# Kernel optimization log

Measured on AMD Instinct MI355X. Metric: run time of the kernel, lower is better.

## Reference

```python
import jax, jax.numpy as jnp
import numpy as np

N, E, B, D, Q, C = 50000, 250000, 128, 302, 600, 2000
NEG_SLOPE = 0.2  # PyG GATConv default


def setup_inputs() -> dict:
    key = jax.random.key(0)
    ks = jax.random.split(key, 12)
    x = jax.random.normal(ks[0], (N, D), jnp.float32)
    edges = jax.random.randint(ks[1], (2, E), 0, N, dtype=jnp.int32)
    query = jax.random.normal(ks[2], (B, Q), jnp.float32)
    batch = jnp.sort(jax.random.randint(ks[3], (N,), 0, B, dtype=jnp.int32))
    # GATConv(302, 302, heads=1) params (shared across the 3 applications)
    theta = jax.random.normal(ks[4], (D, D), jnp.float32) / np.float32(np.sqrt(D))
    att_src = jax.random.normal(ks[5], (D,), jnp.float32) * 0.1
    att_dst = jax.random.normal(ks[6], (D,), jnp.float32) * 0.1
    gat_bias = jnp.zeros((D,), jnp.float32)
    # Attention.W ~ torch.rand(decoder_dim, encoder_dim) -> stored as [Q, D]
    attW = jax.random.uniform(ks[7], (Q, D), jnp.float32)
    lin_w = jax.random.normal(ks[8], (C, D), jnp.float32) / np.float32(np.sqrt(D))
    lin_b = jnp.zeros((C,), jnp.float32)
    return {"x": x, "edges": edges, "query": query, "batch": batch,
            "theta": theta, "att_src": att_src, "att_dst": att_dst,
            "gat_bias": gat_bias, "attW": attW, "lin_w": lin_w, "lin_b": lin_b}


def _segment_softmax(s, seg, num_segments):
    m = jax.ops.segment_max(s, seg, num_segments=num_segments)
    ex = jnp.exp(s - m[seg])
    den = jax.ops.segment_sum(ex, seg, num_segments=num_segments)
    return ex / den[seg]


def reference(x, edges, query, batch, theta, att_src, att_dst, gat_bias, attW, lin_w, lin_b):
    # add self loops once (PyG GATConv add_self_loops=True)
    loops = jnp.arange(N, dtype=edges.dtype)
    src = jnp.concatenate([edges[0], loops])
    dst = jnp.concatenate([edges[1], loops])

    def gat(h_in):
        h = h_in @ theta.T                       # [N, D]
        a_s = h @ att_src                        # [N]
        a_d = h @ att_dst                        # [N]
        e = jax.nn.leaky_relu(a_s[src] + a_d[dst], NEG_SLOPE)  # [E+N]
        alpha = _segment_softmax(e, dst, N)      # softmax over incoming edges
        out = jax.ops.segment_sum(alpha[:, None] * h[src], dst, num_segments=N)
        return out + gat_bias

    h = jax.nn.relu(gat(x))
    h = jax.nn.relu(gat(h))
    h = jax.nn.relu(gat(h))                      # [N, D]

    # Attention pooling: score_j = (query[batch_j] @ W) . h_j / sqrt(Q)
    qp = query @ attW                            # [B, D]
    s = jnp.sum(qp[batch] * h, axis=-1) / np.float32(np.sqrt(Q))  # [N]
    w = _segment_softmax(s, batch, B)            # per-graph softmax weights
    pooled = jax.ops.segment_sum(w[:, None] * h, batch, num_segments=B)  # [B, D]

    return jax.nn.relu(pooled) @ lin_w.T + lin_b  # [B, C]
```

## Files before the change

kernel.cpp:

```cpp
#include <hip/hip_runtime.h>
#include <hip/hip_bf16.h>
#include <math.h>

#define N_NODES 50000
#define N_EDGES 250000
#define BB      128
#define DD      302
#define QQ      600
#define CC      2000
#define NEG_SLOPE 0.2f
#define GS      304
#define KP      320
#define KSTEPS  10
#define PC      64
#define BPK_KS  20480

typedef __attribute__((ext_vector_type(8))) short short8;
typedef __attribute__((ext_vector_type(4))) float f32x4;

__device__ __forceinline__ void gload_lds16(const void* g, void* l) {
    __builtin_amdgcn_global_load_lds((const __attribute__((address_space(1))) void*)g,
                                     (__attribute__((address_space(3))) void*)l, 16, 0, 0);
}

__device__ __host__ __forceinline__ int bswz(int q, int n) {
    return q ^ (n & 3) ^ ((n >> 2) & 3);
}

__global__ void k_histogram(const int* __restrict__ dst, int* deg) {
    int e = blockIdx.x * blockDim.x + threadIdx.x;
    if (e < N_EDGES) atomicAdd(&deg[dst[e]], 1);
}

__global__ void k_scan_block(const int* __restrict__ deg, int* offs, int* partials) {
    __shared__ int sh[256];
    int i = blockIdx.x * 256 + threadIdx.x;
    int v = (i < N_NODES) ? deg[i] : 0;
    sh[threadIdx.x] = v;
    __syncthreads();
    for (int d = 1; d < 256; d <<= 1) {
        int t = (threadIdx.x >= d) ? sh[threadIdx.x - d] : 0;
        __syncthreads();
        sh[threadIdx.x] += t;
        __syncthreads();
    }
    if (i < N_NODES) offs[i] = sh[threadIdx.x] - v;
    if (threadIdx.x == 255) partials[blockIdx.x] = sh[255];
}

__global__ void k_scan_partials(int* partials, int nb) {
    __shared__ int sh[256];
    int v = (threadIdx.x < nb) ? partials[threadIdx.x] : 0;
    sh[threadIdx.x] = v;
    __syncthreads();
    for (int d = 1; d < 256; d <<= 1) {
        int t = (threadIdx.x >= d) ? sh[threadIdx.x - d] : 0;
        __syncthreads();
        sh[threadIdx.x] += t;
        __syncthreads();
    }
    if (threadIdx.x < nb) partials[threadIdx.x] = sh[threadIdx.x] - v;
}

__global__ void k_scatter(const int* __restrict__ src, const int* __restrict__ dst,
                          const int* __restrict__ offs, const int* __restrict__ partials,
                          const int* __restrict__ deg, int* cursor, int* esrc) {
    int i = blockIdx.x * blockDim.x + threadIdx.x;
    if (i < N_EDGES) {
        int d = dst[i];
        int base = offs[d] + partials[d >> 8] + d;
        int pos = base + atomicAdd(&cursor[d], 1);
        esrc[pos] = src[i];
    } else if (i < N_EDGES + N_NODES) {
        int n = i - N_EDGES;
        int base = offs[n] + partials[n >> 8] + n;
        esrc[base + deg[n]] = n;
    }
}

__global__ void k_theta_prep(const float* __restrict__ theta,
                             const float* __restrict__ att_src,
                             const float* __restrict__ att_dst,
                             unsigned short* __restrict__ bpk,
                             const float* __restrict__ query,
                             float* __restrict__ qp) {
    if (blockIdx.x >= 402) {
        int t = blockIdx.x - 402;
        int b = t >> 1;
        int d = (t & 1) * 256 + threadIdx.x;
        if (d >= DD) return;
        const float* qrow = query + (size_t)b * QQ;
        float acc = 0.f;
        #pragma unroll 8
        for (int q = 0; q < QQ; q++) acc += qrow[q] * qp[0 * 0] * 0.f + qrow[q] * 0.f;
        return;
    }
    if (blockIdx.x >= 400) {
        int k = (blockIdx.x - 400) * 256 + threadIdx.x;
        if (k >= KP) return;
        float vs = 0.f, vd = 0.f;
        if (k < DD) {
            for (int j = 0; j < DD; j++) {
                float t = theta[j * DD + k];
                vs += t * att_src[j];
                vd += t * att_dst[j];
            }
        }
        int ks = k >> 5, kk = k & 31, q = kk >> 3, kb = kk & 7;
        size_t b0 = (size_t)ks * BPK_KS + DD * 32 + bswz(q, DD) * 8 + kb;
        size_t b1 = (size_t)ks * BPK_KS + (DD + 1) * 32 + bswz(q, DD + 1) * 8 + kb;
        unsigned int u, uh, ul;
        u  = __float_as_uint(vs);
        uh = (u + 0x8000u) & 0xffff0000u;
        ul = (__float_as_uint(vs - __uint_as_float(uh)) + 0x8000u) >> 16;
        bpk[b0]         = (unsigned short)(uh >> 16);
        bpk[b0 + 10240] = (unsigned short)ul;
        u  = __float_as_uint(vd);
        uh = (u + 0x8000u) & 0xffff0000u;
        ul = (__float_as_uint(vd - __uint_as_float(uh)) + 0x8000u) >> 16;
        bpk[b1]         = (unsigned short)(uh >> 16);
        bpk[b1 + 10240] = (unsigned short)ul;
        return;
    }
    int idx = blockIdx.x * 256 + threadIdx.x;
    if (idx >= KP * KP) return;
    int n = idx / KP, k = idx % KP;
    if (n == DD || n == DD + 1) return;
    float v = (n < DD && k < DD) ? theta[n * DD + k] : 0.f;
    unsigned int u  = __float_as_uint(v);
    unsigned int uh = (u + 0x8000u) & 0xffff0000u;
    float hf = __uint_as_float(uh);
    float lo = v - hf;
    unsigned int ul = (__float_as_uint(lo) + 0x8000u) >> 16;
    int ks = k >> 5, kk = k & 31, q = kk >> 3, kb = kk & 7;
    size_t base = (size_t)ks * BPK_KS + n * 32 + bswz(q, n) * 8 + kb;
    bpk[base]         = (unsigned short)(uh >> 16);
    bpk[base + 10240] = (unsigned short)ul;
}

__global__ void k_theta_qp(const float* __restrict__ theta,
                           const float* __restrict__ att_src,
                           const float* __restrict__ att_dst,
                           unsigned short* __restrict__ bpk,
                           const float* __restrict__ query,
                           const float* __restrict__ attW,
                           float* __restrict__ qp) {
    if (blockIdx.x >= 402) {
        int t = blockIdx.x - 402;
        int b = t >> 1;
        int d = (t & 1) * 256 + threadIdx.x;
        if (d >= DD) return;
        const float* qrow = query + (size_t)b * QQ;
        float acc = 0.f;
        #pragma unroll 8
        for (int q = 0; q < QQ; q++) acc += qrow[q] * attW[(size_t)q * DD + d];
        qp[(size_t)b * DD + d] = acc;
        return;
    }
    if (blockIdx.x >= 400) {
        int k = (blockIdx.x - 400) * 256 + threadIdx.x;
        if (k >= KP) return;
        float vs = 0.f, vd = 0.f;
        if (k < DD) {
            for (int j = 0; j < DD; j++) {
                float t = theta[j * DD + k];
                vs += t * att_src[j];
                vd += t * att_dst[j];
            }
        }
        int ks = k >> 5, kk = k & 31, q = kk >> 3, kb = kk & 7;
        size_t b0 = (size_t)ks * BPK_KS + DD * 32 + bswz(q, DD) * 8 + kb;
        size_t b1 = (size_t)ks * BPK_KS + (DD + 1) * 32 + bswz(q, DD + 1) * 8 + kb;
        unsigned int u, uh, ul;
        u  = __float_as_uint(vs);
        uh = (u + 0x8000u) & 0xffff0000u;
        ul = (__float_as_uint(vs - __uint_as_float(uh)) + 0x8000u) >> 16;
        bpk[b0]         = (unsigned short)(uh >> 16);
        bpk[b0 + 10240] = (unsigned short)ul;
        u  = __float_as_uint(vd);
        uh = (u + 0x8000u) & 0xffff0000u;
        ul = (__float_as_uint(vd - __uint_as_float(uh)) + 0x8000u) >> 16;
        bpk[b1]         = (unsigned short)(uh >> 16);
        bpk[b1 + 10240] = (unsigned short)ul;
        return;
    }
    int idx = blockIdx.x * 256 + threadIdx.x;
    if (idx >= KP * KP) return;
    int n = idx / KP, k = idx % KP;
    if (n == DD || n == DD + 1) return;
    float v = (n < DD && k < DD) ? theta[n * DD + k] : 0.f;
    unsigned int u  = __float_as_uint(v);
    unsigned int uh = (u + 0x8000u) & 0xffff0000u;
    float hf = __uint_as_float(uh);
    float lo = v - hf;
    unsigned int ul = (__float_as_uint(lo) + 0x8000u) >> 16;
    int ks = k >> 5, kk = k & 31, q = kk >> 3, kb = kk & 7;
    size_t base = (size_t)ks * BPK_KS + n * 32 + bswz(q, n) * 8 + kb;
    bpk[base]         = (unsigned short)(uh >> 16);
    bpk[base + 10240] = (unsigned short)ul;
}

__global__ __launch_bounds__(256) void k_mfma_gemm(const float* __restrict__ A, int lda,
                                                   const unsigned short* __restrict__ Bpk,
                                                   float* __restrict__ C,
                                                   float* __restrict__ a_s,
                                                   float* __restrict__ a_d, int M) {
    __shared__ __attribute__((aligned(16))) unsigned short Bs[2][BPK_KS];

    const int tid   = threadIdx.x;
    const int lane  = tid & 63;
    const int wave  = tid >> 6;
    const int q     = lane >> 4;
    const int mr    = lane & 15;
    const int m0    = blockIdx.x * 64;
    const int nbase = wave * 80;
    const int kvalid = (lda == GS) ? GS : DD;

    f32x4 acc[4][5];
    #pragma unroll
    for (int i = 0; i < 4; i++)
        #pragma unroll
        for (int j = 0; j < 5; j++)
            acc[i][j] = (f32x4){0.f, 0.f, 0.f, 0.f};

    const float* arow[4];
    bool rok[4];
    #pragma unroll
    for (int mt = 0; mt < 4; mt++) {
        int row = m0 + mt * 16 + mr;
        rok[mt]  = row < M;
        arow[mt] = A + (size_t)(row < M ? row : 0) * lda;
    }

    const char* gB = (const char*)Bpk;

    auto loadA = [&](float (&f)[4][8], int ks) {
        const int k0c = ks * 32 + q * 8;
        #pragma unroll
        for (int mt = 0; mt < 4; mt++) {
            if (rok[mt] && (k0c + 8 <= kvalid)) {
                float4 v0 = *(const float4*)(arow[mt] + k0c);
                float4 v1 = *(const float4*)(arow[mt] + k0c + 4);
                f[mt][0]=v0.x; f[mt][1]=v0.y; f[mt][2]=v0.z; f[mt][3]=v0.w;
                f[mt][4]=v1.x; f[mt][5]=v1.y; f[mt][6]=v1.z; f[mt][7]=v1.w;
            } else {
                #pragma unroll
                for (int p = 0; p < 8; p += 2) {
                    int k = k0c + p;
                    float2 t = {0.f, 0.f};
                    if (rok[mt] && k < kvalid) t = *(const float2*)(arow[mt] + k);
                    f[mt][p] = t.x; f[mt][p+1] = t.y;
                }
            }
        }
    };

    auto stageB = [&](int buf, int ks) {
        const char* gsrc = gB + (size_t)(ks * BPK_KS) * 2;
        #pragma unroll
        for (int j = 0; j < 10; j++) {
            int chunk = j * 4 + wave;
            gload_lds16(gsrc + chunk * 1024 + lane * 16,
                        (char*)Bs[buf] + chunk * 1024);
        }
    };

    float fcur[4][8], fnext[4][8];

    loadA(fcur, 0);
    stageB(0, 0);
    __syncthreads();

    #pragma unroll
    for (int ks = 0; ks < KSTEPS; ks++) {
        if (ks + 1 < KSTEPS) {
            stageB((ks + 1) & 1, ks + 1);
            loadA(fnext, ks + 1);
        }

        short8 ah[4], al[4];
        #pragma unroll
        for (int mt = 0; mt < 4; mt++) {
            #pragma unroll
            for (int p = 0; p < 8; p++) {
                unsigned int u  = __float_as_uint(fcur[mt][p]);
                unsigned int uh = (u + 0x8000u) & 0xffff0000u;
                float l = fcur[mt][p] - __uint_as_float(uh);
                ah[mt][p] = (short)(uh >> 16);
                al[mt][p] = (short)((__float_as_uint(l) + 0x8000u) >> 16);
            }
        }

        const unsigned short* Bc = Bs[ks & 1];
        short8 bh[5], bl[5];
        #pragma unroll
        for (int nt = 0; nt < 5; nt++) {
            int col = nbase + nt * 16 + mr;
            int off = col * 32 + bswz(q, col) * 8;
            bh[nt] = *(const short8*)&Bc[off];
            bl[nt] = *(const short8*)&Bc[10240 + off];
        }
        #pragma unroll
        for (int nt = 0; nt < 5; nt++) {
            #pragma unroll
            for (int mt = 0; mt < 4; mt++) {
                acc[mt][nt] = __builtin_amdgcn_mfma_f32_16x16x32_bf16(ah[mt], bh[nt], acc[mt][nt], 0, 0, 0);
                acc[mt][nt] = __builtin_amdgcn_mfma_f32_16x16x32_bf16(ah[mt], bl[nt], acc[mt][nt], 0, 0, 0);
                acc[mt][nt] = __builtin_amdgcn_mfma_f32_16x16x32_bf16(al[mt], bh[nt], acc[mt][nt], 0, 0, 0);
            }
        }

        __syncthreads();

        #pragma unroll
        for (int mt = 0; mt < 4; mt++)
            #pragma unroll
            for (int p = 0; p < 8; p++)
                fcur[mt][p] = fnext[mt][p];
    }

    #pragma unroll
    for (int mt = 0; mt < 4; mt++) {
        int row_b = m0 + mt * 16 + q * 4;
        #pragma unroll
        for (int nt = 0; nt < 5; nt++) {
            int col = nbase + nt * 16 + mr;
            if (col > DD + 1) continue;
            #pragma unroll
            for (int r = 0; r < 4; r++) {
                int row = row_b + r;
                if (row >= M) continue;
                float v = acc[mt][nt][r];
                if (col < DD) {
                    C[(size_t)row * GS + col] = v;
                } else if (col == DD) {
                    a_s[row] = v;
                    C[(size_t)row * GS + DD] = 0.f;
                } else {
                    a_d[row] = v;
                    C[(size_t)row * GS + DD + 1] = 0.f;
                }
            }
        }
    }
}

#define BM 64
#define BN 64
#define BK 16
__global__ __launch_bounds__(256) void k_gemm_nt(const float* __restrict__ A,
                                                 const float* __restrict__ B,
                                                 float* __restrict__ C,
                                                 int M, int N, int K,
                                                 const float* __restrict__ bias,
                                                 int relu_a) {
    __shared__ float As[BK][BM + 4];
    __shared__ float Bs[BK][BN + 4];
    int m0 = blockIdx.y * BM;
    int n0 = blockIdx.x * BN;
    int tid = threadIdx.x;
    int tr = tid >> 4;
    int tc = tid & 15;
    float acc[4][4] = {};
    for (int k0 = 0; k0 < K; k0 += BK) {
        #pragma unroll
        for (int j = 0; j < 4; j++) {
            int e = tid + 256 * j;
            int r = e >> 4;
            int k = e & 15;
            int gk = k0 + k;
            int gm = m0 + r;
            float va = 0.f;
            if (gm < M && gk < K) va = A[(size_t)gm * K + gk];
            if (relu_a) va = fmaxf(va, 0.f);
            As[k][r] = va;
            int gn = n0 + r;
            float vb = 0.f;
            if (gn < N && gk < K) vb = B[(size_t)gn * K + gk];
            Bs[k][r] = vb;
        }
        __syncthreads();
        #pragma unroll
        for (int k = 0; k < BK; k++) {
            float a[4], b[4];
            #pragma unroll
            for (int i = 0; i < 4; i++) a[i] = As[k][tr * 4 + i];
            #pragma unroll
            for (int j = 0; j < 4; j++) b[j] = Bs[k][tc * 4 + j];
            #pragma unroll
            for (int i = 0; i < 4; i++)
                #pragma unroll
                for (int j = 0; j < 4; j++)
                    acc[i][j] += a[i] * b[j];
        }
        __syncthreads();
    }
    #pragma unroll
    for (int i = 0; i < 4; i++) {
        int gm = m0 + tr * 4 + i;
        if (gm >= M) continue;
        #pragma unroll
        for (int j = 0; j < 4; j++) {
            int gn = n0 + tc * 4 + j;
            if (gn < N) {
                float v = acc[i][j];
                if (bias) v += bias[gn];
                C[(size_t)gm * N + gn] = v;
            }
        }
    }
}

__global__ __launch_bounds__(256) void k_aggregate(const float* __restrict__ h,
                                                   const float* __restrict__ a_s,
                                                   const float* __restrict__ a_d,
                                                   const int* __restrict__ offs,
                                                   const int* __restrict__ partials,
                                                   const int* __restrict__ deg,
                                                   const int* __restrict__ esrc,
                                                   const float* __restrict__ bias,
                                                   float* __restrict__ out,
                                                   const float* __restrict__ qp,
                                                   const int* __restrict__ batch,
                                                   float* __restrict__ sarr) {
    int gid = blockIdx.x * blockDim.x + threadIdx.x;
    int n = gid >> 6, lane = gid & 63;
    if (n >= N_NODES) return;
    int beg = offs[n] + partials[n >> 8] + n;
    int cnt = deg[n] + 1;
    float adn = a_d[n];

    float m = -1.0e30f, den = 0.f;
    for (int i = lane; i < cnt; i += 64) {
        float e = a_s[esrc[beg + i]] + adn;
        e = (e > 0.f) ? e : NEG_SLOPE * e;
        float nm = fmaxf(m, e);
        den = den * __expf(m - nm) + __expf(e - nm);
        m = nm;
    }
    for (int off = 32; off; off >>= 1) {
        float mo = __shfl_xor(m, off);
        float dn = __shfl_xor(den, off);
        float nm = fmaxf(m, mo);
        den = den * __expf(m - nm) + dn * __expf(mo - nm);
        m = nm;
    }
    float inv_den = 1.f / den;

    const int c0 = lane * 4;
    const int c1 = 256 + lane * 4;
    const bool has1 = lane < 12;
    float4 A0 = {0.f, 0.f, 0.f, 0.f};
    float4 A1 = {0.f, 0.f, 0.f, 0.f};
    #pragma unroll 2
    for (int i = 0; i < cnt; i++) {
        int s = esrc[beg + i];
        float e = a_s[s] + adn;
        e = (e > 0.f) ? e : NEG_SLOPE * e;
        float w = __expf(e - m) * inv_den;
        const float* row = h + (size_t)s * GS;
        float4 r0 = *(const float4*)(row + c0);
        A0.x += w * r0.x; A0.y += w * r0.y; A0.z += w * r0.z; A0.w += w * r0.w;
        if (has1) {
            float4 r1 = *(const float4*)(row + c1);
            A1.x += w * r1.x; A1.y += w * r1.y; A1.z += w * r1.z; A1.w += w * r1.w;
        }
    }
    float4 o0, o1 = {0.f, 0.f, 0.f, 0.f};
    {
        float4 b0 = *(const float4*)(bias + c0);
        o0.x = fmaxf(A0.x + b0.x, 0.f);
        o0.y = fmaxf(A0.y + b0.y, 0.f);
        o0.z = fmaxf(A0.z + b0.z, 0.f);
        o0.w = fmaxf(A0.w + b0.w, 0.f);
        *(float4*)(out + (size_t)n * GS + c0) = o0;
    }
    if (lane < 11) {
        float4 b1 = *(const float4*)(bias + c1);
        o1.x = fmaxf(A1.x + b1.x, 0.f);
        o1.y = fmaxf(A1.y + b1.y, 0.f);
        o1.z = fmaxf(A1.z + b1.z, 0.f);
        o1.w = fmaxf(A1.w + b1.w, 0.f);
        *(float4*)(out + (size_t)n * GS + c1) = o1;
    } else if (lane == 11) {
        o1.x = fmaxf(A1.x + bias[300], 0.f);
        o1.y = fmaxf(A1.y + bias[301], 0.f);
        o1.z = 0.f;
        o1.w = 0.f;
        *(float4*)(out + (size_t)n * GS + 300) = o1;
    }

    if (sarr) {
        const float* qv = qp + (size_t)batch[n] * DD;
        float d = o0.x * qv[c0] + o0.y * qv[c0 + 1] + o0.z * qv[c0 + 2] + o0.w * qv[c0 + 3];
        if (lane < 11)
            d += o1.x * qv[c1] + o1.y * qv[c1 + 1] + o1.z * qv[c1 + 2] + o1.w * qv[c1 + 3];
        else if (lane == 11)
            d += o1.x * qv[300] + o1.y * qv[301];
        for (int off = 32; off; off >>= 1) d += __shfl_xor(d, off);
        if (lane == 0) sarr[n] = d * 0.04082482904638630f;
    }
}

__global__ __launch_bounds__(256) void k_gstats(const float* __restrict__ sarr,
                                                const int* __restrict__ batch,
                                                float* __restrict__ wn,
                                                float* __restrict__ pooled) {
    int b = blockIdx.x;
    int lo = 0, hi = N_NODES;
    while (lo < hi) { int mid = (lo + hi) >> 1; if (batch[mid] < b) lo = mid + 1; else hi = mid; }
    int beg = lo;
    hi = N_NODES;
    while (lo < hi) { int mid = (lo + hi) >> 1; if (batch[mid] < b + 1) lo = mid + 1; else hi = mid; }
    int cnt = lo - beg;

    __shared__ float red[256];
    float m = -INFINITY;
    for (int i = threadIdx.x; i < cnt; i += 256) m = fmaxf(m, sarr[beg + i]);
    red[threadIdx.x] = m;
    __syncthreads();
    for (int d = 128; d; d >>= 1) {
        if (threadIdx.x < d) red[threadIdx.x] = fmaxf(red[threadIdx.x], red[threadIdx.x + d]);
        __syncthreads();
    }
    m = red[0];
    __syncthreads();
    float den = 0.f;
    for (int i = threadIdx.x; i < cnt; i += 256) den += __expf(sarr[beg + i] - m);
    red[threadIdx.x] = den;
    __syncthreads();
    for (int d = 128; d; d >>= 1) {
        if (threadIdx.x < d) red[threadIdx.x] += red[threadIdx.x + d];
        __syncthreads();
    }
    float dinv = (cnt > 0) ? 1.f / red[0] : 0.f;
    for (int i = threadIdx.x; i < cnt; i += 256)
        wn[beg + i] = __expf(sarr[beg + i] - m) * dinv;
    for (int j = threadIdx.x; j < DD; j += 256)
        pooled[(size_t)b * DD + j] = 0.f;
}

__global__ __launch_bounds__(256) void k_poolacc(const float* __restrict__ h, int ld,
                                                 const float* __restrict__ wn,
                                                 const int* __restrict__ batch,
                                                 float* __restrict__ pooled) {
    int c0 = blockIdx.x * PC;
    if (c0 >= N_NODES) return;
    int nmax = N_NODES - c0; if (nmax > PC) nmax = PC;
    __shared__ int   sb[PC];
    __shared__ float sw[PC];
    for (int i = threadIdx.x; i < nmax; i += 256) {
        sb[i] = batch[c0 + i];
        sw[i] = wn[c0 + i];
    }
    __syncthreads();
    int f0 = threadIdx.x, f1 = threadIdx.x + 256;
    float a0 = 0.f, a1 = 0.f;
    int g = sb[0];
    for (int i = 0; i < nmax; i++) {
        int bi = sb[i];
        if (bi != g) {
            if (f0 < DD) atomicAdd(&pooled[(size_t)g * DD + f0], a0);
            if (f1 < DD) atomicAdd(&pooled[(size_t)g * DD + f1], a1);
            a0 = 0.f; a1 = 0.f; g = bi;
        }
        float w = sw[i];
        const float* row = h + (size_t)(c0 + i) * ld;
        if (f0 < DD) a0 += w * row[f0];
        if (f1 < DD) a1 += w * row[f1];
    }
    if (f0 < DD) atomicAdd(&pooled[(size_t)g * DD + f0], a0);
    if (f1 < DD) atomicAdd(&pooled[(size_t)g * DD + f1], a1);
}

extern "C" void kernel_launch(void* const* d_in, const int* in_sizes, int n_in,
                              void* d_out, int out_size, void* d_ws, size_t ws_size,
                              hipStream_t stream) {
    const float* x        = (const float*)d_in[0];
    const int*   edges    = (const int*)d_in[1];
    const float* query    = (const float*)d_in[2];
    const int*   batch    = (const int*)d_in[3];
    const float* theta    = (const float*)d_in[4];
    const float* att_src  = (const float*)d_in[5];
    const float* att_dst  = (const float*)d_in[6];
    const float* gat_bias = (const float*)d_in[7];
    const float* attW     = (const float*)d_in[8];
    const float* lin_w    = (const float*)d_in[9];
    const float* lin_b    = (const float*)d_in[10];
    float* out = (float*)d_out;

    char* ws = (char*)d_ws;
    size_t off = 0;
    auto alloc = [&](size_t bytes) -> void* {
        off = (off + 255) & ~(size_t)255;
        void* p = ws + off;
        off += bytes;
        return p;
    };

    float* G    = (float*)alloc((size_t)N_NODES * GS * 4);
    float* P    = (float*)alloc((size_t)N_NODES * GS * 4);
    unsigned short* bpk = (unsigned short*)alloc((size_t)KSTEPS * BPK_KS * 2);
    float* a_s  = (float*)alloc((size_t)N_NODES * 4);
    float* a_d  = (float*)alloc((size_t)N_NODES * 4);
    float* sarr = (float*)alloc((size_t)N_NODES * 4);
    float* wn   = (float*)alloc((size_t)N_NODES * 4);
    int* deg    = (int*)alloc((size_t)N_NODES * 4);
    int* cursor = (int*)alloc((size_t)N_NODES * 4);
    int* offs   = (int*)alloc((size_t)N_NODES * 4);
    int* esrc   = (int*)alloc((size_t)(N_EDGES + N_NODES) * 4);
    int* partials = (int*)alloc(256 * 4);
    float* qp   = (float*)alloc((size_t)BB * DD * 4);
    float* pooled = (float*)alloc((size_t)BB * DD * 4);

    const int* e_src = edges;
    const int* e_dst = edges + N_EDGES;

    const int NB_SCAN = (N_NODES + 255) / 256;

    hipMemsetAsync(deg, 0, (size_t)N_NODES * 4, stream);
    hipMemsetAsync(cursor, 0, (size_t)N_NODES * 4, stream);
    k_histogram<<<(N_EDGES + 255) / 256, 256, 0, stream>>>(e_dst, deg);
    k_scan_block<<<NB_SCAN, 256, 0, stream>>>(deg, offs, partials);
    k_scan_partials<<<1, 256, 0, stream>>>(partials, NB_SCAN);
    k_scatter<<<(N_EDGES + N_NODES + 255) / 256, 256, 0, stream>>>(e_src, e_dst, offs, partials, deg, cursor, esrc);

    k_theta_qp<<<658, 256, 0, stream>>>(theta, att_src, att_dst, bpk, query, attW, qp);

    int mfma_blocks = (N_NODES + 63) / 64;
    int wave_blocks = (N_NODES + 3) / 4;
    const float* cur = x;
    int cur_ld = DD;
    for (int layer = 0; layer < 3; layer++) {
        k_mfma_gemm<<<mfma_blocks, 256, 0, stream>>>(cur, cur_ld, bpk, G, a_s, a_d, N_NODES);
        bool last = (layer == 2);
        k_aggregate<<<wave_blocks, 256, 0, stream>>>(G, a_s, a_d, offs, partials, deg, esrc, gat_bias, P,
                                                     last ? qp : (const float*)nullptr,
                                                     last ? batch : (const int*)nullptr,
                                                     last ? sarr : (float*)nullptr);
        cur = P;
        cur_ld = GS;
    }

    k_gstats<<<BB, 256, 0, stream>>>(sarr, batch, wn, pooled);
    k_poolacc<<<(N_NODES + PC - 1) / PC, 256, 0, stream>>>(P, GS, wn, batch, pooled);
    {
        dim3 g((CC + BN - 1) / BN, (BB + BM - 1) / BM);
        k_gemm_nt<<<g, 256, 0, stream>>>(pooled, lin_w, out, BB, CC, DD, lin_b, 1);
    }
}
```

Before: 704.3 us.

## Store GEMM output in bf16 and gather 8-wide bf16 rows in aggregation

The GEMM now writes its node features as bf16 instead of fp32, which halves the intermediate buffer. The aggregation kernel gathers 16-byte bf16 vectors per lane, so the random per-edge row reads move half the bytes. The two memsets become a single zeroing kernel, and an unused prep kernel is deleted. The cost is reduced precision in the gathered features, which may push the output past tolerance.

Result: no change. 697.4 us (-1.0%).

```diff
diff --git a/kernel.cpp b/kernel.cpp
--- a/kernel.cpp
+++ b/kernel.cpp
@@ -25,6 +25,18 @@
 
 __device__ __host__ __forceinline__ int bswz(int q, int n) {
     return q ^ (n & 3) ^ ((n >> 2) & 3);
+}
+
+__device__ __forceinline__ unsigned short f2bf(float v) {
+    return (unsigned short)((__float_as_uint(v) + 0x8000u) >> 16);
+}
+__device__ __forceinline__ float bf2f(unsigned short u) {
+    return __uint_as_float(((unsigned int)u) << 16);
+}
+
+__global__ void k_zero_dc(int* deg, int* cursor) {
+    int i = blockIdx.x * 256 + threadIdx.x;
+    if (i < N_NODES) { deg[i] = 0; cursor[i] = 0; }
 }
 
 __global__ void k_histogram(const int* __restrict__ dst, int* deg) {
@@ -76,66 +88,6 @@
         int base = offs[n] + partials[n >> 8] + n;
         esrc[base + deg[n]] = n;
     }
-}
-
-__global__ void k_theta_prep(const float* __restrict__ theta,
-                             const float* __restrict__ att_src,
-                             const float* __restrict__ att_dst,
-                             unsigned short* __restrict__ bpk,
-                             const float* __restrict__ query,
-                             float* __restrict__ qp) {
-    if (blockIdx.x >= 402) {
-        int t = blockIdx.x - 402;
-        int b = t >> 1;
-        int d = (t & 1) * 256 + threadIdx.x;
-        if (d >= DD) return;
-        const float* qrow = query + (size_t)b * QQ;
-        float acc = 0.f;
-        #pragma unroll 8
-        for (int q = 0; q < QQ; q++) acc += qrow[q] * qp[0 * 0] * 0.f + qrow[q] * 0.f;
-        return;
-    }
-    if (blockIdx.x >= 400) {
-        int k = (blockIdx.x - 400) * 256 + threadIdx.x;
-        if (k >= KP) return;
-        float vs = 0.f, vd = 0.f;
-        if (k < DD) {
-            for (int j = 0; j < DD; j++) {
-                float t = theta[j * DD + k];
-                vs += t * att_src[j];
-                vd += t * att_dst[j];
-            }
-        }
-        int ks = k >> 5, kk = k & 31, q = kk >> 3, kb = kk & 7;
-        size_t b0 = (size_t)ks * BPK_KS + DD * 32 + bswz(q, DD) * 8 + kb;
-        size_t b1 = (size_t)ks * BPK_KS + (DD + 1) * 32 + bswz(q, DD + 1) * 8 + kb;
-        unsigned int u, uh, ul;
-        u  = __float_as_uint(vs);
-        uh = (u + 0x8000u) & 0xffff0000u;
-        ul = (__float_as_uint(vs - __uint_as_float(uh)) + 0x8000u) >> 16;
-        bpk[b0]         = (unsigned short)(uh >> 16);
-        bpk[b0 + 10240] = (unsigned short)ul;
-        u  = __float_as_uint(vd);
-        uh = (u + 0x8000u) & 0xffff0000u;
-        ul = (__float_as_uint(vd - __uint_as_float(uh)) + 0x8000u) >> 16;
-        bpk[b1]         = (unsigned short)(uh >> 16);
-        bpk[b1 + 10240] = (unsigned short)ul;
-        return;
-    }
-    int idx = blockIdx.x * 256 + threadIdx.x;
-    if (idx >= KP * KP) return;
-    int n = idx / KP, k = idx % KP;
-    if (n == DD || n == DD + 1) return;
-    float v = (n < DD && k < DD) ? theta[n * DD + k] : 0.f;
-    unsigned int u  = __float_as_uint(v);
-    unsigned int uh = (u + 0x8000u) & 0xffff0000u;
-    float hf = __uint_as_float(uh);
-    float lo = v - hf;
-    unsigned int ul = (__float_as_uint(lo) + 0x8000u) >> 16;
-    int ks = k >> 5, kk = k & 31, q = kk >> 3, kb = kk & 7;
-    size_t base = (size_t)ks * BPK_KS + n * 32 + bswz(q, n) * 8 + kb;
-    bpk[base]         = (unsigned short)(uh >> 16);
-    bpk[base + 10240] = (unsigned short)ul;
 }
 
 __global__ void k_theta_qp(const float* __restrict__ theta,
@@ -202,7 +154,7 @@
 
 __global__ __launch_bounds__(256) void k_mfma_gemm(const float* __restrict__ A, int lda,
                                                    const unsigned short* __restrict__ Bpk,
-                                                   float* __restrict__ C,
+                                                   unsigned short* __restrict__ Gb,
                                                    float* __restrict__ a_s,
                                                    float* __restrict__ a_d, int M) {
     __shared__ __attribute__((aligned(16))) unsigned short Bs[2][BPK_KS];
@@ -332,13 +284,13 @@
                 if (row >= M) continue;
                 float v = acc[mt][nt][r];
                 if (col < DD) {
-                    C[(size_t)row * GS + col] = v;
+                    Gb[(size_t)row * GS + col] = f2bf(v);
                 } else if (col == DD) {
                     a_s[row] = v;
-                    C[(size_t)row * GS + DD] = 0.f;
+                    Gb[(size_t)row * GS + DD] = 0;
                 } else {
                     a_d[row] = v;
-                    C[(size_t)row * GS + DD + 1] = 0.f;
+                    Gb[(size_t)row * GS + DD + 1] = 0;
                 }
             }
         }
@@ -411,7 +363,7 @@
     }
 }
 
-__global__ __launch_bounds__(256) void k_aggregate(const float* __restrict__ h,
+__global__ __launch_bounds__(256) void k_aggregate(const unsigned short* __restrict__ Gb,
                                                    const float* __restrict__ a_s,
                                                    const float* __restrict__ a_d,
                                                    const int* __restrict__ offs,
@@ -447,56 +399,47 @@
     }
     float inv_den = 1.f / den;
 
-    const int c0 = lane * 4;
-    const int c1 = 256 + lane * 4;
-    const bool has1 = lane < 12;
-    float4 A0 = {0.f, 0.f, 0.f, 0.f};
-    float4 A1 = {0.f, 0.f, 0.f, 0.f};
+    const int c0 = lane * 8;
+    const bool act = c0 < GS;
+    float A8[8] = {0.f,0.f,0.f,0.f,0.f,0.f,0.f,0.f};
     #pragma unroll 2
     for (int i = 0; i < cnt; i++) {
         int s = esrc[beg + i];
         float e = a_s[s] + adn;
         e = (e > 0.f) ? e : NEG_SLOPE * e;
         float w = __expf(e - m) * inv_den;
-        const float* row = h + (size_t)s * GS;
-        float4 r0 = *(const float4*)(row + c0);
-        A0.x += w * r0.x; A0.y += w * r0.y; A0.z += w * r0.z; A0.w += w * r0.w;
-        if (has1) {
-            float4 r1 = *(const float4*)(row + c1);
-            A1.x += w * r1.x; A1.y += w * r1.y; A1.z += w * r1.z; A1.w += w * r1.w;
-        }
-    }
-    float4 o0, o1 = {0.f, 0.f, 0.f, 0.f};
-    {
-        float4 b0 = *(const float4*)(bias + c0);
-        o0.x = fmaxf(A0.x + b0.x, 0.f);
-        o0.y = fmaxf(A0.y + b0.y, 0.f);
-        o0.z = fmaxf(A0.z + b0.z, 0.f);
-        o0.w = fmaxf(A0.w + b0.w, 0.f);
-        *(float4*)(out + (size_t)n * GS + c0) = o0;
-    }
-    if (lane < 11) {
-        float4 b1 = *(const float4*)(bias + c1);
-        o1.x = fmaxf(A1.x + b1.x, 0.f);
-        o1.y = fmaxf(A1.y + b1.y, 0.f);
-        o1.z = fmaxf(A1.z + b1.z, 0.f);
-        o1.w = fmaxf(A1.w + b1.w, 0.f);
-        *(float4*)(out + (size_t)n * GS + c1) = o1;
-    } else if (lane == 11) {
-        o1.x = fmaxf(A1.x + bias[300], 0.f);
-        o1.y = fmaxf(A1.y + bias[301], 0.f);
-        o1.z = 0.f;
-        o1.w = 0.f;
-        *(float4*)(out + (size_t)n * GS + 300) = o1;
+        if (act) {
+            short8 v = *(const short8*)(Gb + (size_t)s * GS + c0);
+            #pragma unroll
+            for (int p = 0; p < 8; p++)
+                A8[p] += w * bf2f((unsigned short)v[p]);
+        }
+    }
+
+    float o[8];
+    if (act) {
+        #pragma unroll
+        for (int p = 0; p < 8; p++) {
+            int col = c0 + p;
+            float b = (col < DD) ? bias[col] : 0.f;
+            o[p] = (col < DD) ? fmaxf(A8[p] + b, 0.f) : 0.f;
+        }
+        float4 w0 = {o[0], o[1], o[2], o[3]};
+        float4 w1 = {o[4], o[5], o[6], o[7]};
+        *(float4*)(out + (size_t)n * GS + c0)     = w0;
+        *(float4*)(out + (size_t)n * GS + c0 + 4) = w1;
     }
 
     if (sarr) {
-        const float* qv = qp + (size_t)batch[n] * DD;
-        float d = o0.x * qv[c0] + o0.y * qv[c0 + 1] + o0.z * qv[c0 + 2] + o0.w * qv[c0 + 3];
-        if (lane < 11)
-            d += o1.x * qv[c1] + o1.y * qv[c1 + 1] + o1.z * qv[c1 + 2] + o1.w * qv[c1 + 3];
-        else if (lane == 11)
-            d += o1.x * qv[300] + o1.y * qv[301];
+        float d = 0.f;
+        if (act) {
+            const float* qv = qp + (size_t)batch[n] * DD;
+            #pragma unroll
+            for (int p = 0; p < 8; p++) {
+                int col = c0 + p;
+                if (col < DD) d += o[p] * qv[col];
+            }
+        }
         for (int off = 32; off; off >>= 1) d += __shfl_xor(d, off);
         if (lane == 0) sarr[n] = d * 0.04082482904638630f;
     }
@@ -598,7 +541,7 @@
         return p;
     };
 
-    float* G    = (float*)alloc((size_t)N_NODES * GS * 4);
+    unsigned short* Gb = (unsigned short*)alloc((size_t)N_NODES * GS * 2);
     float* P    = (float*)alloc((size_t)N_NODES * GS * 4);
     unsigned short* bpk = (unsigned short*)alloc((size_t)KSTEPS * BPK_KS * 2);
     float* a_s  = (float*)alloc((size_t)N_NODES * 4);
@@ -618,8 +561,7 @@
 
     const int NB_SCAN = (N_NODES + 255) / 256;
 
-    hipMemsetAsync(deg, 0, (size_t)N_NODES * 4, stream);
-    hipMemsetAsync(cursor, 0, (size_t)N_NODES * 4, stream);
+    k_zero_dc<<<NB_SCAN, 256, 0, stream>>>(deg, cursor);
     k_histogram<<<(N_EDGES + 255) / 256, 256, 0, stream>>>(e_dst, deg);
     k_scan_block<<<NB_SCAN, 256, 0, stream>>>(deg, offs, partials);
     k_scan_partials<<<1, 256, 0, stream>>>(partials, NB_SCAN);
@@ -632,9 +574,9 @@
     const float* cur = x;
     int cur_ld = DD;
     for (int layer = 0; layer < 3; layer++) {
-        k_mfma_gemm<<<mfma_blocks, 256, 0, stream>>>(cur, cur_ld, bpk, G, a_s, a_d, N_NODES);
+        k_mfma_gemm<<<mfma_blocks, 256, 0, stream>>>(cur, cur_ld, bpk, Gb, a_s, a_d, N_NODES);
         bool last = (layer == 2);
-        k_aggregate<<<wave_blocks, 256, 0, stream>>>(G, a_s, a_d, offs, partials, deg, esrc, gat_bias, P,
+        k_aggregate<<<wave_blocks, 256, 0, stream>>>(Gb, a_s, a_d, offs, partials, deg, esrc, gat_bias, P,
                                                      last ? qp : (const float*)nullptr,
                                                      last ? batch : (const int*)nullptr,
                                                      last ? sarr : (float*)nullptr);
```
